# Optimization experiments

Hardware: AMD Instinct MI355X
Metric: run time of the kernel (lower is better)

The kernel has to match this reference:

```python
import jax, jax.numpy as jnp
import numpy as np

NUM_CLASSES = 81
THRESHOLD = 0.5
NEGPOS_RATIO = 3
VARIANCE = (0.1, 0.2)
B, P, O = 32, 24564, 50


def point_form(pr):
    # center-form (cx,cy,w,h) -> corner-form (x1,y1,x2,y2)
    return jnp.concatenate([pr[:, :2] - pr[:, 2:] / 2, pr[:, :2] + pr[:, 2:] / 2], axis=1)


def jaccard(a, b):
    # a: [O,4] corner-form truths, b: [P,4] corner-form priors -> [O,P]
    lt = jnp.maximum(a[:, None, :2], b[None, :, :2])
    rb = jnp.minimum(a[:, None, 2:], b[None, :, 2:])
    wh = jnp.clip(rb - lt, 0.0)
    inter = wh[..., 0] * wh[..., 1]
    area_a = ((a[:, 2] - a[:, 0]) * (a[:, 3] - a[:, 1]))[:, None]
    area_b = ((b[:, 2] - b[:, 0]) * (b[:, 3] - b[:, 1]))[None, :]
    return inter / (area_a + area_b - inter)


def encode(matched, priors_cf):
    # matched: [P,4] corner-form gt; priors_cf: [P,4] center-form
    g_cxcy = ((matched[:, :2] + matched[:, 2:]) / 2 - priors_cf[:, :2]) / (VARIANCE[0] * priors_cf[:, 2:])
    g_wh = jnp.log((matched[:, 2:] - matched[:, :2]) / priors_cf[:, 2:]) / VARIANCE[1]
    return jnp.concatenate([g_cxcy, g_wh], axis=1)


def match_one(truths, labels, priors_cf, priors_pf):
    ov = jaccard(truths, priors_pf)                       # [O,P]
    best_prior_idx = jnp.argmax(ov, axis=1)               # [O] best prior per truth
    best_truth_overlap = jnp.max(ov, axis=0)              # [P]
    best_truth_idx = jnp.argmax(ov, axis=0)               # [P]
    # ensure every gt matches its best prior
    best_truth_overlap = best_truth_overlap.at[best_prior_idx].set(2.0)
    best_truth_idx = best_truth_idx.at[best_prior_idx].set(jnp.arange(truths.shape[0]))
    matches = truths[best_truth_idx]                      # [P,4]
    conf = labels[best_truth_idx] + 1                     # background = 0
    conf = jnp.where(best_truth_overlap < THRESHOLD, 0, conf)
    loc = encode(matches, priors_cf)
    return loc, conf


def setup_inputs() -> dict:
    key = jax.random.key(0)
    k1, k2, k3, k4, k5, k6, k7 = jax.random.split(key, 7)
    loc_data = jax.random.normal(k1, (B, P, 4), jnp.float32)
    conf_data = jax.random.normal(k2, (B, P, NUM_CLASSES), jnp.float32)
    cxcy = jax.random.uniform(k3, (P, 2), minval=0.05, maxval=0.95)
    wh = jax.random.uniform(k4, (P, 2), minval=0.05, maxval=0.5)
    priors = jnp.concatenate([cxcy, wh], axis=1).astype(jnp.float32)
    gc = jax.random.uniform(k5, (B, O, 2), minval=0.1, maxval=0.9)
    gwh = jax.random.uniform(k6, (B, O, 2), minval=0.05, maxval=0.4)
    boxes = jnp.clip(jnp.concatenate([gc - gwh / 2, gc + gwh / 2], axis=-1), 0.0, 1.0)
    labels = jax.random.randint(k7, (B, O), 0, NUM_CLASSES - 1).astype(jnp.float32)
    targets = jnp.concatenate([boxes, labels[..., None]], axis=-1).astype(jnp.float32)
    return {"loc_data": loc_data, "conf_data": conf_data, "priors": priors, "targets": targets}


def reference(loc_data, conf_data, priors, targets):
    truths = targets[..., :4]                              # [B,O,4]
    labels = targets[..., 4].astype(jnp.int32)             # [B,O]
    priors_pf = point_form(priors)
    loc_t, conf_t = jax.vmap(match_one, in_axes=(0, 0, None, None))(truths, labels, priors, priors_pf)
    pos = conf_t > 0                                       # [B,P]

    # localization smooth-L1 over positives (sum reduction)
    diff = loc_data - loc_t
    sl1 = jnp.where(jnp.abs(diff) < 1.0, 0.5 * diff * diff, jnp.abs(diff) - 0.5)
    loss_l = jnp.sum(sl1 * pos[..., None].astype(sl1.dtype))

    # per-anchor CE loss for hard negative mining
    lse = jax.nn.logsumexp(conf_data, axis=-1)             # [B,P]
    gathered = jnp.take_along_axis(conf_data, conf_t[..., None], axis=-1)[..., 0]
    loss_c_all = lse - gathered                            # [B,P]
    loss_c_mine = jnp.where(pos, 0.0, loss_c_all)
    loss_idx = jnp.argsort(-loss_c_mine, axis=1)
    idx_rank = jnp.argsort(loss_idx, axis=1)
    num_pos = jnp.sum(pos.astype(jnp.int32), axis=1, keepdims=True)  # [B,1]
    num_neg = jnp.minimum(NEGPOS_RATIO * num_pos, P - 1)
    neg = idx_rank < num_neg                               # [B,P]

    sel = jnp.logical_or(pos, neg)
    loss_c = jnp.sum(jnp.where(sel, loss_c_all, 0.0))

    N = jnp.sum(num_pos).astype(loss_l.dtype)
    return loss_l / N, loss_c / N
```

## Files before the change

kernel.cpp:

```cpp
#include <hip/hip_runtime.h>

#define NB 32
#define NP 24564
#define NO 50
#define NC 81
#define THR 0.5f
#define KA_CHUNK 1024
#define NCH 24

__device__ __forceinline__ float rl_f(float v, int j) {
  return __uint_as_float((unsigned)__builtin_amdgcn_readlane((int)__float_as_uint(v), j));
}
__device__ __forceinline__ float bp_f(float v, int j4) {
  return __uint_as_float((unsigned)__builtin_amdgcn_ds_bpermute(j4, (int)__float_as_uint(v)));
}


__global__ __launch_bounds__(256) void kA(
    const float* __restrict__ priors, const float* __restrict__ targets,
    unsigned long long* __restrict__ bpc,
    double* __restrict__ acc, int* __restrict__ num_pos,
    float* __restrict__ accLb, float* __restrict__ accCb,
    int* __restrict__ done) {
  __shared__ float4 s_pf[KA_CHUNK];
  __shared__ float s_t[NO * 5];
  __shared__ unsigned long long s_bp[256];
  const int b = blockIdx.y;
  const int tid = threadIdx.x;
  const int base = blockIdx.x * KA_CHUNK;

  if (blockIdx.x == 0 && b == 0) {
    if (tid < 4) acc[tid] = 0.0;
    else if (tid >= 32 && tid < 64) num_pos[tid - 32] = 0;
    else if (tid >= 64 && tid < 96) accLb[tid - 64] = 0.0f;
    else if (tid >= 96 && tid < 128) accCb[tid - 96] = 0.0f;
    else if (tid == 128) *done = 0;
  }

  for (int i = tid; i < NO * 5; i += 256) s_t[i] = targets[b * NO * 5 + i];

  #pragma unroll
  for (int k = 0; k < KA_CHUNK / 256; ++k) {
    const int p = base + k * 256 + tid;
    float4 pf;
    if (p < NP) {
      const float4 pr = ((const float4*)priors)[p];
      pf = make_float4(pr.x - pr.z * 0.5f, pr.y - pr.w * 0.5f,
                       pr.x + pr.z * 0.5f, pr.y + pr.w * 0.5f);
    } else {
      pf = make_float4(3.0f, 3.0f, 3.0f, 3.0f);
    }
    s_pf[k * 256 + tid] = pf;
  }
  __syncthreads();

  const int wv = tid >> 6;
  const int lane = tid & 63;
  unsigned long long best = 0ull;
  if (lane < NO) {
    const float tx1 = s_t[lane * 5 + 0], ty1 = s_t[lane * 5 + 1];
    const float tx2 = s_t[lane * 5 + 2], ty2 = s_t[lane * 5 + 3];
    const float area_a = (tx2 - tx1) * (ty2 - ty1);
    const int i0 = wv * 256;
    #pragma unroll 8
    for (int i = 0; i < 256; ++i) {
      const float4 q = s_pf[i0 + i];
      const float wx = fmaxf(fminf(q.z, tx2) - fmaxf(q.x, tx1), 0.0f);
      const float wy = fmaxf(fminf(q.w, ty2) - fmaxf(q.y, ty1), 0.0f);
      const float inter = wx * wy;
      const float ab = (q.z - q.x) * (q.w - q.y);
      const float iou = __fdividef(inter, area_a + ab - inter);
      const unsigned p = (unsigned)(base + i0 + i);
      const unsigned long long pk =
          (((unsigned long long)__float_as_uint(iou)) << 32) |
          (unsigned long long)(0xFFFFFFFFu - p);
      if (pk > best) best = pk;
    }
  }
  s_bp[tid] = best;
  __syncthreads();
  if (tid < NO) {
    unsigned long long m = s_bp[tid];
    unsigned long long v = s_bp[64 + tid];  if (v > m) m = v;
    v = s_bp[128 + tid];                    if (v > m) m = v;
    v = s_bp[192 + tid];                    if (v > m) m = v;
    bpc[(size_t)blockIdx.x * (NB * NO) + b * NO + tid] = m;
  }
}

__global__ __launch_bounds__(512) void kMS(
    const float* __restrict__ loc, const float* __restrict__ conf,
    const float* __restrict__ priors, const float* __restrict__ targets,
    const unsigned long long* __restrict__ bpc,
    float* __restrict__ mine, int* __restrict__ num_pos,
    float* __restrict__ accLb, float* __restrict__ accCb) {
  __shared__ float s_s[512];
  __shared__ int s_tpb[NO];
  __shared__ float sLw[8], sCw[8];
  __shared__ int sNw[8];

  const int tid = threadIdx.x;
  const int lane = tid & 63;
  const int b = blockIdx.y;
  const int rowbase = blockIdx.x * 512 + (tid & ~63);
  const int p = rowbase + lane;
  const bool valid = (p < NP);
  const int pc = valid ? p : NP - 1;
  const size_t grow = (size_t)b * NP + pc;
  const float* tb = targets + (size_t)b * (NO * 5);

  if (tid < NO) {
    unsigned long long m = 0ull;
    #pragma unroll
    for (int c = 0; c < NCH; ++c) {
      const unsigned long long v = bpc[(size_t)c * (NB * NO) + b * NO + tid];
      if (v > m) m = v;
    }
    s_tpb[tid] = (int)(0xFFFFFFFFu - (unsigned)(m & 0xFFFFFFFFull));
  }

  float ttx1 = 3.f, tty1 = 3.f, ttx2 = 3.f, tty2 = 3.f, tar = 0.f, tlab = 0.f;
  if (lane < NO) {
    ttx1 = tb[lane * 5 + 0]; tty1 = tb[lane * 5 + 1];
    ttx2 = tb[lane * 5 + 2]; tty2 = tb[lane * 5 + 3];
    tlab = tb[lane * 5 + 4];
    tar = (ttx2 - ttx1) * (tty2 - tty1);
  }
  const float4 pr = ((const float4*)priors)[pc];
  const float4 ldv = ((const float4*)loc)[grow];
  const float px1 = pr.x - pr.z * 0.5f, py1 = pr.y - pr.w * 0.5f;
  const float px2 = pr.x + pr.z * 0.5f, py2 = pr.y + pr.w * 0.5f;
  const float areab = (px2 - px1) * (py2 - py1);
  __syncthreads();
  const int tpb = (lane < NO) ? s_tpb[lane] : -1;

  const int l16 = lane & 15;
  const int g4 = (lane >> 4) & 3;
  const int c0 = (4 - g4) & 3;
  const int tc = (l16 < c0) ? l16 : (c0 + 64 + (l16 - c0));
  const float* cb = conf + (size_t)b * NP * NC;

  float4 v4[8];
  float vta[8], v80[8];

  #define KMS_ROWP(ph) (cb + (size_t)((rowbase + (ph) * 4 + g4) < NP \
      ? (rowbase + (ph) * 4 + g4) : (NP - 1)) * NC)
  #define KMS_ISSUE(ph) { const float* rp_ = KMS_ROWP(ph);            \
      v4[(ph) & 7] = *(const float4*)(rp_ + c0 + 4 * l16);            \
      vta[(ph) & 7] = rp_[tc]; v80[(ph) & 7] = rp_[80]; }

  KMS_ISSUE(0) KMS_ISSUE(1) KMS_ISSUE(2)
  KMS_ISSUE(3) KMS_ISSUE(4) KMS_ISSUE(5)
  __builtin_amdgcn_sched_barrier(0);

  float bv = -1.0f;
  int bj = 0;
  #pragma unroll 2
  for (int j = 0; j < NO; ++j) {
    const float x1 = rl_f(ttx1, j), y1 = rl_f(tty1, j);
    const float x2 = rl_f(ttx2, j), y2 = rl_f(tty2, j);
    const float aa = rl_f(tar, j);
    const float wx = fmaxf(fminf(x2, px2) - fmaxf(x1, px1), 0.0f);
    const float wy = fmaxf(fminf(y2, py2) - fmaxf(y1, py1), 0.0f);
    const float inter = wx * wy;
    const float iou = __fdividef(inter, aa + areab - inter);
    if (iou > bv) { bv = iou; bj = j; }
  }

  int ovj = -1;
  unsigned long long M = __ballot((lane < NO) && ((unsigned)(tpb - rowbase) < 64u));
  while (M) {
    const int l = __ffsll((long long)M) - 1;
    M &= M - 1;
    const int r = __builtin_amdgcn_readlane(tpb, l) - rowbase;
    if (lane == r) ovj = l;
  }
  const int jm = (ovj >= 0) ? ovj : bj;
  const bool pos = valid && ((ovj >= 0) || (bv >= THR));
  const int j4 = jm << 2;
  const float lab = bp_f(tlab, j4);
  const float mx1 = bp_f(ttx1, j4), my1 = bp_f(tty1, j4);
  const float mx2 = bp_f(ttx2, j4), my2 = bp_f(tty2, j4);
  const int conft = pos ? ((int)lab + 1) : 0;

  const float gval = conf[grow * NC + conft];

  float sl1 = 0.0f;
  if (pos) {
    const float gcx = __fdividef((mx1 + mx2) * 0.5f - pr.x, 0.1f * pr.z);
    const float gcy = __fdividef((my1 + my2) * 0.5f - pr.y, 0.1f * pr.w);
    const float gw = __logf(__fdividef(mx2 - mx1, pr.z)) * 5.0f;
    const float gh = __logf(__fdividef(my2 - my1, pr.w)) * 5.0f;
    const float d0 = ldv.x - gcx, d1 = ldv.y - gcy;
    const float d2 = ldv.z - gw, d3 = ldv.w - gh;
    #pragma unroll
    for (int q = 0; q < 4; ++q) {
      const float d = (q == 0) ? d0 : (q == 1) ? d1 : (q == 2) ? d2 : d3;
      const float a = fabsf(d);
      sl1 += (a < 1.0f) ? 0.5f * d * d : a - 0.5f;
    }
  }

  #pragma unroll
  for (int ph = 0; ph < 16; ++ph) {
    if (ph + 6 < 16) KMS_ISSUE(ph + 6)
    const float4 v = v4[ph & 7];
    float s = __expf(v.x) + __expf(v.y) + __expf(v.z) + __expf(v.w);
    s += __expf(vta[ph & 7]);
    const float e80 = __expf(v80[ph & 7]);
    s += (l16 == 0) ? e80 : 0.0f;
    s += __shfl_xor(s, 1, 64);
    s += __shfl_xor(s, 2, 64);
    s += __shfl_xor(s, 4, 64);
    s += __shfl_xor(s, 8, 64);
    if (l16 == 0) s_s[(tid & ~63) + ph * 4 + g4] = s;
  }
  const float myS = s_s[tid];

  const float lca = __logf(myS) - gval;

  float sumL = 0.0f, sumC = 0.0f;
  int cnt = 0;
  if (valid) {
    mine[grow] = pos ? 0.0f : fmaxf(lca, 0.0f);
    if (pos) { cnt = 1; sumC = lca; sumL = sl1; }
  }

  #pragma unroll
  for (int m = 1; m <= 32; m <<= 1) {
    sumL += __shfl_xor(sumL, m, 64);
    sumC += __shfl_xor(sumC, m, 64);
    cnt  += __shfl_xor(cnt, m, 64);
  }
  const int w = tid >> 6;
  if (lane == 0) { sLw[w] = sumL; sCw[w] = sumC; sNw[w] = cnt; }
  __syncthreads();
  if (tid == 0) {
    float L = 0.0f, C = 0.0f;
    int n = 0;
    #pragma unroll
    for (int q = 0; q < 8; ++q) { L += sLw[q]; C += sCw[q]; n += sNw[q]; }
    if (L != 0.0f) atomicAdd(&accLb[b], L);
    if (C != 0.0f) atomicAdd(&accCb[b], C);
    if (n) atomicAdd(&num_pos[b], n);
  }
}

__global__ __launch_bounds__(512) void kD(
    const float* __restrict__ mine, const int* __restrict__ num_pos,
    double* __restrict__ acc, int* __restrict__ done,
    const float* __restrict__ accLb, const float* __restrict__ accCb,
    float* __restrict__ out) {
  const int b = blockIdx.x;
  const int tid = threadIdx.x;
  const uint4* vb4 = (const uint4*)(mine + (size_t)b * NP);

  unsigned vals[48];
  #pragma unroll
  for (int k = 0; k < 12; ++k) {
    const int i = tid + k * 512;
    uint4 q = make_uint4(0u, 0u, 0u, 0u);
    if (i < NP / 4) q = vb4[i];
    vals[4 * k + 0] = q.x; vals[4 * k + 1] = q.y;
    vals[4 * k + 2] = q.z; vals[4 * k + 3] = q.w;
  }

  const int K = min(3 * num_pos[b], NP - 1);

  __shared__ int s_w[2][8];
  unsigned prefix = 0u;
  int remaining = K;

  for (int bit = 30; bit >= 0; --bit) {
    const unsigned want = (prefix >> bit) | 1u;
    int cnt = 0;
    #pragma unroll
    for (int k = 0; k < 48; ++k) cnt += ((vals[k] >> bit) == want) ? 1 : 0;
    #pragma unroll
    for (int m = 32; m >= 1; m >>= 1) cnt += __shfl_xor(cnt, m, 64);
    const int buf = bit & 1;
    if ((tid & 63) == 0) s_w[buf][tid >> 6] = cnt;
    __syncthreads();
    int total = 0;
    #pragma unroll
    for (int w = 0; w < 8; ++w) total += s_w[buf][w];
    if (total >= remaining) prefix |= (1u << bit);
    else remaining -= total;
  }

  if (K > 0) {
    const float t = __uint_as_float(prefix);
    double sg = 0.0;
    int cg = 0;
    #pragma unroll
    for (int k = 0; k < 48; ++k) {
      const float f = __uint_as_float(vals[k]);
      if (f > t) { sg += (double)f; cg++; }
    }
    #pragma unroll
    for (int m = 32; m >= 1; m >>= 1) {
      sg += __shfl_xor(sg, m, 64);
      cg += __shfl_xor(cg, m, 64);
    }
    __shared__ double s_sd[8];
    __shared__ int s_sc[8];
    const int wid = tid >> 6;
    if ((tid & 63) == 0) { s_sd[wid] = sg; s_sc[wid] = cg; }
    __syncthreads();
    if (tid == 0) {
      double S = 0.0;
      int C = 0;
      for (int w = 0; w < 8; ++w) { S += s_sd[w]; C += s_sc[w]; }
      S += (double)(K - C) * (double)t;
      atomicAdd(&acc[2], S);
    }
  }

  __shared__ int s_last;
  __syncthreads();
  if (tid == 0) {
    __threadfence();
    s_last = (atomicAdd(done, 1) == NB - 1) ? 1 : 0;
  }
  __syncthreads();
  if (s_last && tid < 64) {
    __threadfence();
    int n = 0;
    float L = 0.0f, C = 0.0f;
    if (tid < NB) { n = num_pos[tid]; L = accLb[tid]; C = accCb[tid]; }
    #pragma unroll
    for (int m = 32; m >= 1; m >>= 1) {
      n += __shfl_xor(n, m, 64);
      L += __shfl_xor(L, m, 64);
      C += __shfl_xor(C, m, 64);
    }
    if (tid == 0) {
      const double S = atomicAdd(&acc[2], 0.0);
      const double Nf = (double)n;
      out[0] = (float)((double)L / Nf);
      out[1] = (float)(((double)C + S) / Nf);
    }
  }
}

extern "C" void kernel_launch(void* const* d_in, const int* in_sizes, int n_in,
                              void* d_out, int out_size, void* d_ws, size_t ws_size,
                              hipStream_t stream) {
  const float* loc     = (const float*)d_in[0];
  const float* conf    = (const float*)d_in[1];
  const float* priors  = (const float*)d_in[2];
  const float* targets = (const float*)d_in[3];
  float* out = (float*)d_out;

  char* ws = (char*)d_ws;
  double* acc   = (double*)ws;
  int* num_pos  = (int*)(ws + 32);
  float* accLb  = (float*)(ws + 160);
  float* accCb  = (float*)(ws + 288);
  int* done     = (int*)(ws + 416);
  unsigned long long* bpc = (unsigned long long*)(ws + 552);
  const size_t hdr = 307760;
  float* mine  = (float*)(ws + hdr);

  dim3 gA(NCH, NB);
  kA<<<gA, 256, 0, stream>>>(priors, targets, bpc,
                             acc, num_pos, accLb, accCb, done);

  dim3 gM((NP + 511) / 512, NB);
  kMS<<<gM, 512, 0, stream>>>(loc, conf, priors, targets, bpc,
                              mine, num_pos, accLb, accCb);

  kD<<<NB, 512, 0, stream>>>(mine, num_pos, acc, done, accLb, accCb, out);
}
```

Baseline: 145.7 us.

## Stage conf rows into LDS via async global_load_lds double buffering

Replaces the per-lane register loads of conf rows in the match/softmax kernel with direct global-to-LDS DMA, staging 8 rows per wave into a double-buffered shared tile while the previous tile is reduced. The gathered target-class logit is now read from LDS instead of a separate scattered global load. The aim is coalesced contiguous loads and overlap of memory with exp/sum work. In exchange it adds about 48KB of LDS per block, which may cut occupancy, and relies on manual vmcnt waits without a barrier between waves, so ordering errors could break correctness.

```diff
diff --git a/kernel.cpp b/kernel.cpp
--- a/kernel.cpp
+++ b/kernel.cpp
@@ -94,6 +94,7 @@
     const unsigned long long* __restrict__ bpc,
     float* __restrict__ mine, int* __restrict__ num_pos,
     float* __restrict__ accLb, float* __restrict__ accCb) {
+  __shared__ float s_dma[8][2][768];
   __shared__ float s_s[512];
   __shared__ int s_tpb[NO];
   __shared__ float sLw[8], sCw[8];
@@ -101,8 +102,9 @@
 
   const int tid = threadIdx.x;
   const int lane = tid & 63;
+  const int w = tid >> 6;
   const int b = blockIdx.y;
-  const int rowbase = blockIdx.x * 512 + (tid & ~63);
+  const int rowbase = blockIdx.x * 512 + w * 64;
   const int p = rowbase + lane;
   const bool valid = (p < NP);
   const int pc = valid ? p : NP - 1;
@@ -134,24 +136,23 @@
   __syncthreads();
   const int tpb = (lane < NO) ? s_tpb[lane] : -1;
 
-  const int l16 = lane & 15;
-  const int g4 = (lane >> 4) & 3;
-  const int c0 = (4 - g4) & 3;
-  const int tc = (l16 < c0) ? l16 : (c0 + 64 + (l16 - c0));
-  const float* cb = conf + (size_t)b * NP * NC;
-
-  float4 v4[8];
-  float vta[8], v80[8];
-
-  #define KMS_ROWP(ph) (cb + (size_t)((rowbase + (ph) * 4 + g4) < NP \
-      ? (rowbase + (ph) * 4 + g4) : (NP - 1)) * NC)
-  #define KMS_ISSUE(ph) { const float* rp_ = KMS_ROWP(ph);            \
-      v4[(ph) & 7] = *(const float4*)(rp_ + c0 + 4 * l16);            \
-      vta[(ph) & 7] = rp_[tc]; v80[(ph) & 7] = rp_[80]; }
-
-  KMS_ISSUE(0) KMS_ISSUE(1) KMS_ISSUE(2)
-  KMS_ISSUE(3) KMS_ISSUE(4) KMS_ISSUE(5)
-  __builtin_amdgcn_sched_barrier(0);
+  const unsigned* confu = (const unsigned*)conf;
+  const size_t total_dw = (size_t)NB * NP * NC;
+  const size_t max_dw = total_dw - 4;
+  auto stage = [&](int bufsel, int t) {
+    const size_t tile_dw = ((size_t)b * NP + (size_t)(rowbase + t * 8)) * NC;
+    #pragma unroll
+    for (int s = 0; s < 3; ++s) {
+      size_t idx = tile_dw + (size_t)(s * 256 + lane * 4);
+      if (idx > max_dw) idx = max_dw;
+      __builtin_amdgcn_global_load_lds(
+          (const __attribute__((address_space(1))) unsigned*)(confu + idx),
+          (__attribute__((address_space(3))) unsigned*)(&s_dma[w][bufsel][s * 256]),
+          16, 0, 0);
+    }
+  };
+
+  stage(0, 0);
 
   float bv = -1.0f;
   int bj = 0;
@@ -183,8 +184,6 @@
   const float mx2 = bp_f(ttx2, j4), my2 = bp_f(tty2, j4);
   const int conft = pos ? ((int)lab + 1) : 0;
 
-  const float gval = conf[grow * NC + conft];
-
   float sl1 = 0.0f;
   if (pos) {
     const float gcx = __fdividef((mx1 + mx2) * 0.5f - pr.x, 0.1f * pr.z);
@@ -201,19 +200,36 @@
     }
   }
 
-  #pragma unroll
-  for (int ph = 0; ph < 16; ++ph) {
-    if (ph + 6 < 16) KMS_ISSUE(ph + 6)
-    const float4 v = v4[ph & 7];
-    float s = __expf(v.x) + __expf(v.y) + __expf(v.z) + __expf(v.w);
-    s += __expf(vta[ph & 7]);
-    const float e80 = __expf(v80[ph & 7]);
-    s += (l16 == 0) ? e80 : 0.0f;
+  const int r8 = lane >> 3;
+  const int l8 = lane & 7;
+  float gval = 0.0f;
+  #pragma unroll 2
+  for (int t = 0; t < 8; ++t) {
+    if (t + 1 < 8) {
+      stage((t + 1) & 1, t + 1);
+      asm volatile("s_waitcnt vmcnt(3)" ::: "memory");
+    } else {
+      asm volatile("s_waitcnt vmcnt(0)" ::: "memory");
+    }
+    __builtin_amdgcn_sched_barrier(0);
+    const float* buf = &s_dma[w][t & 1][0];
+    const float* rowp = buf + r8 * 81;
+    int kk = r8;
+    float a0 = 0.0f, a1 = 0.0f;
+    #pragma unroll
+    for (int k = 0; k < 10; ++k) {
+      const int c = l8 + 8 * kk;
+      const float e = __expf(rowp[c]);
+      if (k & 1) a1 += e; else a0 += e;
+      kk = (kk == 9) ? 0 : kk + 1;
+    }
+    float s = a0 + a1;
+    if (l8 == 0) s += __expf(rowp[80]);
     s += __shfl_xor(s, 1, 64);
     s += __shfl_xor(s, 2, 64);
     s += __shfl_xor(s, 4, 64);
-    s += __shfl_xor(s, 8, 64);
-    if (l16 == 0) s_s[(tid & ~63) + ph * 4 + g4] = s;
+    if (l8 == 0) s_s[w * 64 + t * 8 + r8] = s;
+    if (r8 == t) gval = buf[l8 * 81 + conft];
   }
   const float myS = s_s[tid];
 
@@ -232,7 +248,6 @@
     sumC += __shfl_xor(sumC, m, 64);
     cnt  += __shfl_xor(cnt, m, 64);
   }
-  const int w = tid >> 6;
   if (lane == 0) { sLw[w] = sumL; sCw[w] = sumC; sNw[w] = cnt; }
   __syncthreads();
   if (tid == 0) {
```

Result: faster. 142.7 us (median of 2 runs) (-2.1%).
